# Kernel tuning notes

Measured on AMD Instinct MI355X. Metric: run time of the kernel, lower is better.

Reference implementation:

```python
import jax, jax.numpy as jnp
import numpy as np

B, L, V, E, H, DOUT = 32, 128, 30000, 300, 512, 5
NUM_STEPS = 5
WINDOW = 1


def setup_inputs() -> dict:
    key = jax.random.key(0)
    ks = jax.random.split(key, 16)
    def p(k, shape, scale=0.02):
        return jax.random.normal(k, shape, jnp.float32) * scale
    tokens = jax.random.randint(ks[0], (B, L), 1, V)
    lengths = jnp.maximum(jax.random.randint(ks[1], (B,), 1, L + 1), 8)
    embed = p(ks[2], (V, E), 0.1).at[0].set(0.0)  # padding_idx=0 row zeroed
    W0 = p(ks[3], (E, H)); b0 = jnp.zeros((H,), jnp.float32)
    Wg = p(ks[4], (3 * H + E + H, 7 * H)); bg = jnp.zeros((7 * H,), jnp.float32)
    Wgf = p(ks[5], (2 * H, H)); bgf = jnp.zeros((H,), jnp.float32)
    Wfi = p(ks[6], (2 * H, H)); bfi = jnp.zeros((H,), jnp.float32)
    Wgo = p(ks[7], (2 * H, H)); bgo = jnp.zeros((H,), jnp.float32)
    W1 = p(ks[8], (H, 2 * H)); b1 = jnp.zeros((2 * H,), jnp.float32)
    W2 = p(ks[9], (2 * H, DOUT)); b2 = jnp.zeros((DOUT,), jnp.float32)
    return dict(tokens=tokens, lengths=lengths, embed=embed, W0=W0, b0=b0,
                Wg=Wg, bg=bg, Wgf=Wgf, bgf=bgf, Wfi=Wfi, bfi=bfi,
                Wgo=Wgo, bgo=bgo, W1=W1, b1=b1, W2=W2, b2=b2)


def _shift_r(a, k):  # h_{i-k}
    return jnp.pad(a, ((0, 0), (k, 0), (0, 0)))[:, :L]


def _shift_l(a, k):  # h_{i+k}
    return jnp.pad(a, ((0, 0), (0, k), (0, 0)))[:, k:]


def reference(tokens, lengths, embed, W0, b0, Wg, bg, Wgf, bgf, Wfi, bfi,
              Wgo, bgo, W1, b1, W2, b2):
    x = embed[tokens]                                   # [B,L,E]
    mask = (jnp.arange(L)[None, :] < lengths[:, None]).astype(x.dtype)[:, :, None]
    lens = jnp.maximum(lengths.astype(x.dtype), 1.0)[:, None]  # [B,1]
    h = jnp.tanh(x @ W0 + b0) * mask                    # word node init [B,L,H]
    c = jnp.zeros_like(h)
    g = jnp.sum(h, axis=1) / lens                       # global node [B,H]
    cg = jnp.zeros_like(g)

    def step(carry, _):
        h, c, g, cg = carry
        hl = sum(_shift_r(h, k) for k in range(1, WINDOW + 1))
        hr = sum(_shift_l(h, k) for k in range(1, WINDOW + 1))
        gb = jnp.broadcast_to(g[:, None, :], h.shape)
        ctx = jnp.concatenate([hl, h, hr, x, gb], axis=-1)  # [B,L,3H+E+H]
        gates = ctx @ Wg + bg                               # [B,L,7H]
        gi, gl, gf, gr, gs, go, gu = jnp.split(gates, 7, axis=-1)
        nrm = jax.nn.softmax(jnp.stack([gi, gl, gf, gr, gs], 0), axis=0)
        i_, l_, f_, r_, s_ = nrm[0], nrm[1], nrm[2], nrm[3], nrm[4]
        o = jax.nn.sigmoid(go)
        u = jnp.tanh(gu)
        c_new = (l_ * _shift_r(c, 1) + f_ * c + r_ * _shift_l(c, 1)
                 + s_ * cg[:, None, :] + i_ * u) * mask
        h_new = o * jnp.tanh(c_new) * mask
        # global (sentence-state) node update
        h_avg = jnp.sum(h_new, axis=1) / lens
        gcat = jnp.concatenate([g, h_avg], axis=-1)         # [B,2H]
        fg = gcat @ Wgf + bgf                               # [B,H]
        og = jax.nn.sigmoid(gcat @ Wgo + bgo)
        fi = jnp.concatenate([jnp.broadcast_to(g[:, None, :], h_new.shape),
                              h_new], axis=-1) @ Wfi + bfi  # [B,L,H]
        slot_logits = jnp.concatenate([fg[:, None, :], fi], axis=1)  # [B,L+1,H]
        slot_mask = jnp.concatenate([jnp.ones((B, 1, 1), x.dtype), mask], axis=1)
        slot_logits = jnp.where(slot_mask > 0, slot_logits, -1e9)
        w = jax.nn.softmax(slot_logits, axis=1)
        cg_new = w[:, 0] * cg + jnp.sum(w[:, 1:] * c_new, axis=1)
        g_new = og * jnp.tanh(cg_new)
        return (h_new, c_new, g_new, cg_new), None

    (h, c, g, cg), _ = jax.lax.scan(step, (h, c, g, cg), None, length=NUM_STEPS)
    logits = jnp.tanh(g @ W1 + b1) @ W2 + b2            # [B,DOUT]
    return jax.nn.log_softmax(logits, axis=-1)
```

## Files before the change

### kernel.cpp

```cpp
#include <hip/hip_runtime.h>
#include <hip/hip_bf16.h>
#include <math.h>

#define B_ 32
#define L_ 128
#define LP 130
#define E_ 300
#define EP 320
#define H_ 512
#define DOUT_ 5
#define NSTEP 5
#define G7 3584
#define KGATES 1856
#define KFI 512

typedef __hip_bfloat16 bf16;
using bf16x8 = __attribute__((ext_vector_type(8))) __bf16;
using f32x4 = __attribute__((ext_vector_type(4))) float;

__device__ __forceinline__ void gload16(const void* g, void* l) {
  __builtin_amdgcn_global_load_lds(
      (const __attribute__((address_space(1))) void*)g,
      (__attribute__((address_space(3))) void*)l, 16, 0, 0);
}

__global__ void fill_zero(float* __restrict__ p, int n) {
  int i = blockIdx.x * blockDim.x + threadIdx.x;
  if (i < n) p[i] = 0.f;
}

__global__ void mask_lens_kernel(const int* __restrict__ lengths,
                                 float* __restrict__ maskf,
                                 float* __restrict__ invlens) {
  int i = blockIdx.x * blockDim.x + threadIdx.x;
  if (i < B_ * L_) {
    int b = i >> 7, l = i & 127;
    maskf[i] = (l < lengths[b]) ? 1.f : 0.f;
    if (l == 0) invlens[b] = 1.f / fmaxf((float)lengths[b], 1.f);
  }
}

__global__ void embed_bf16_kernel(const int* __restrict__ tokens,
                                  const float* __restrict__ embed,
                                  bf16* __restrict__ xb) {
  int i = blockIdx.x * blockDim.x + threadIdx.x;
  if (i >= B_ * L_ * EP) return;
  int e = i % EP, bl = i / EP;
  float v = (e < E_) ? embed[(size_t)tokens[bl] * E_ + e] : 0.f;
  xb[i] = __float2bfloat16(v);
}

__global__ void fill_pad(bf16* __restrict__ hpad) {
  int i = blockIdx.x * blockDim.x + threadIdx.x;
  if (i >= B_ * 2 * H_) return;
  int hh = i & (H_ - 1);
  int r = (i >> 9) & 1, b = i >> 10;
  hpad[((size_t)(b * LP + r * (LP - 1))) * H_ + hh] = __float2bfloat16(0.f);
}

__global__ __launch_bounds__(256) void transpose_to_bf16(
    const float* __restrict__ W, bf16* __restrict__ Wt, int Kreal, int Ncols,
    int dstStride) {
  __shared__ float tile[64][65];
  const int k0 = blockIdx.x * 64, n0 = blockIdx.y * 64;
  const int t = threadIdx.x;
  const int nn = t & 63, kk0 = t >> 6;
#pragma unroll
  for (int p = 0; p < 16; ++p) {
    int kk = kk0 + p * 4;
    int gk = k0 + kk;
    tile[kk][nn] = (gk < Kreal) ? W[(size_t)gk * Ncols + n0 + nn] : 0.f;
  }
  __syncthreads();
#pragma unroll
  for (int p = 0; p < 2; ++p) {
    int r = (t >> 3) + p * 32;
    int kb = (t & 7) * 8;
    union { ushort h[8]; uint4 v; } u;
#pragma unroll
    for (int e = 0; e < 8; ++e) {
      bf16 b = __float2bfloat16(tile[kb + e][r]);
      u.h[e] = *(ushort*)&b;
    }
    *(uint4*)&Wt[(size_t)(n0 + r) * dstStride + k0 + kb] = u.v;
  }
}

template <int AMAP, int OUTMODE>
__global__ __launch_bounds__(256) void gemm_mfma(
    const bf16* __restrict__ A, const bf16* __restrict__ X3,
    const bf16* __restrict__ Bt, const float* __restrict__ bias,
    const float* __restrict__ b2batch, const float* __restrict__ rowscale,
    void* __restrict__ Cout, int N, int KP, int act) {
  __shared__ ushort As[128 * 64];
  __shared__ ushort Bs[128 * 64];
  const int tid = threadIdx.x;
  const int lane = tid & 63;
  const int w = tid >> 6;
  const int wr = w >> 1, wc = w & 1;
  const int nbx = gridDim.x;
  const int nwg = nbx * gridDim.y;
  int id = blockIdx.y * nbx + blockIdx.x;
  if ((nwg & 7) == 0) { int q = nwg >> 3; id = (id & 7) * q + (id >> 3); }
  const int bxi = id % nbx, byi = id / nbx;
  const int rowBase = byi * 128, colBase = bxi * 128;
  const int l15 = lane & 15, l4 = lane >> 4;
  f32x4 acc[4][4] = {};

  const bf16* bP[4];
  const bf16* aP[4];
  const bf16* xP[4];
#pragma unroll
  for (int i = 0; i < 4; ++i) {
    int c = tid + 256 * i;
    int r = c >> 3;
    int ql = (c & 7) ^ (r & 7);
    bP[i] = Bt + (size_t)(colBase + r) * KP + ql * 8;
    if constexpr (AMAP == 0) {
      aP[i] = A + (size_t)(rowBase + r) * KP + ql * 8;
    } else {
      const int b = rowBase >> 7;
      aP[i] = A + ((size_t)(b * LP + r)) * H_ + ql * 8;
      xP[i] = X3 + (size_t)(rowBase + r) * EP + ql * 8;
    }
  }

  auto step_ = [&](const bf16* const* ap, int ko, int kb) {
#pragma unroll
    for (int i = 0; i < 4; ++i) {
      gload16(ap[i] + ko, &As[(tid + 256 * i) * 8]);
      gload16(bP[i] + kb, &Bs[(tid + 256 * i) * 8]);
    }
    __syncthreads();
#pragma unroll
    for (int kh = 0; kh < 2; ++kh) {
      bf16x8 aF[4], bF[4];
#pragma unroll
      for (int m = 0; m < 4; ++m) {
        int row = wr * 64 + m * 16 + l15;
        aF[m] = *(const bf16x8*)&As[row * 64 +
                                    (((kh << 2) + l4) ^ (l15 & 7)) * 8];
      }
#pragma unroll
      for (int n = 0; n < 4; ++n) {
        int row = wc * 64 + n * 16 + l15;
        bF[n] = *(const bf16x8*)&Bs[row * 64 +
                                    (((kh << 2) + l4) ^ (l15 & 7)) * 8];
      }
#pragma unroll
      for (int m = 0; m < 4; ++m)
#pragma unroll
        for (int n = 0; n < 4; ++n)
          acc[m][n] = __builtin_amdgcn_mfma_f32_16x16x32_bf16(
              aF[m], bF[n], acc[m][n], 0, 0, 0);
    }
    __syncthreads();
  };

  if constexpr (AMAP == 0) {
    const int nIter = KP >> 6;
    for (int t = 0; t < nIter; ++t) step_(aP, t * 64, t * 64);
  } else {
    for (int t = 0; t < 24; ++t) step_(aP, t * 64, t * 64);
    for (int t = 24; t < 29; ++t) step_(xP, (t - 24) * 64, t * 64);
  }

  const int bidx = rowBase >> 7;
#pragma unroll
  for (int m = 0; m < 4; ++m) {
#pragma unroll
    for (int n = 0; n < 4; ++n) {
      int col = colBase + wc * 64 + n * 16 + l15;
      float bv = bias[col];
      if (b2batch) bv += b2batch[(size_t)bidx * N + col];
      if constexpr (OUTMODE == 5) {
        bf16 tmp[4];
#pragma unroll
        for (int j = 0; j < 4; ++j)
          tmp[j] = __float2bfloat16(acc[m][n][j] + bv);
        int row0 = rowBase + wr * 64 + m * 16 + l4 * 4;
        *(uint2*)&((bf16*)Cout)[((size_t)(row0 >> 2) * N + col) * 4] =
            *(uint2*)tmp;
      } else {
#pragma unroll
        for (int j = 0; j < 4; ++j) {
          int row = rowBase + wr * 64 + m * 16 + l4 * 4 + j;
          float v = acc[m][n][j] + bv;
          if (act == 1) v = tanhf(v);
          v *= rowscale[row];
          size_t oi = ((size_t)((row >> 7) * LP + (row & 127) + 1)) * H_ + col;
          ((bf16*)Cout)[oi] = __float2bfloat16(v);
        }
      }
    }
  }
}

__global__ __launch_bounds__(256) void gvec_gemm(
    const float* __restrict__ g, const float* __restrict__ Wgg,
    const float* __restrict__ Wfi, float* __restrict__ gg,
    float* __restrict__ gfi) {
  __shared__ float vin[H_];
  __shared__ float red[4][64];
  const int b = blockIdx.y;
  for (int i = threadIdx.x; i < H_; i += 256) vin[i] = g[(size_t)b * H_ + i];
  __syncthreads();
  const int o = threadIdx.x & 63, kp = threadIdx.x >> 6;
  const bool isg = blockIdx.x < 56;
  const int n0 = isg ? blockIdx.x * 64 : (blockIdx.x - 56) * 64;
  const float* W = isg ? Wgg : Wfi;
  const int ldw = isg ? G7 : H_;
  float acc = 0.f;
#pragma unroll 4
  for (int k = kp * 128; k < kp * 128 + 128; ++k)
    acc = fmaf(vin[k], W[(size_t)k * ldw + n0 + o], acc);
  red[kp][o] = acc;
  __syncthreads();
  if (threadIdx.x < 64) {
    int t = threadIdx.x;
    float v = red[0][t] + red[1][t] + red[2][t] + red[3][t];
    if (isg) gg[(size_t)b * G7 + n0 + t] = v;
    else gfi[(size_t)b * H_ + n0 + t] = v;
  }
}

__global__ __launch_bounds__(256) void fi_slot_kernel(
    const bf16* __restrict__ hpad, const bf16* __restrict__ Wfit,
    const float* __restrict__ bfi, const float* __restrict__ gfi,
    const float* __restrict__ fg, const float* __restrict__ og,
    const float* __restrict__ c_new, const float* __restrict__ cg_old,
    const float* __restrict__ maskf, float* __restrict__ cg_new,
    float* __restrict__ g_new) {
  __shared__ __align__(16) char smem[64 * 129 * 4 + 3072];
  ushort* As = (ushort*)smem;
  ushort* Bs = As + 128 * 64;
  float* sfi = (float*)smem;
  float* part = sfi + 64 * 129;

  const int tid = threadIdx.x;
  const int lane = tid & 63;
  const int w = tid >> 6;
  const int b = blockIdx.y;
  const int colBase = blockIdx.x * 64;
  const int l15 = lane & 15, l4 = lane >> 4;
  f32x4 acc[2][4] = {};

  const bf16* aP[4];
  const bf16* bP[2];
#pragma unroll
  for (int i = 0; i < 4; ++i) {
    int c = tid + 256 * i;
    int r = c >> 3;
    int ql = (c & 7) ^ (r & 7);
    aP[i] = hpad + ((size_t)(b * LP + r + 1)) * H_ + ql * 8;
  }
#pragma unroll
  for (int i = 0; i < 2; ++i) {
    int c = tid + 256 * i;
    int r = c >> 3;
    int ql = (c & 7) ^ (r & 7);
    bP[i] = Wfit + (size_t)(colBase + r) * KFI + ql * 8;
  }

  for (int t = 0; t < 8; ++t) {
    int k0 = t * 64;
#pragma unroll
    for (int i = 0; i < 4; ++i)
      gload16(aP[i] + k0, &As[(tid + 256 * i) * 8]);
#pragma unroll
    for (int i = 0; i < 2; ++i)
      gload16(bP[i] + k0, &Bs[(tid + 256 * i) * 8]);
    __syncthreads();
#pragma unroll
    for (int kh = 0; kh < 2; ++kh) {
      bf16x8 aF[2], bF[4];
#pragma unroll
      for (int m = 0; m < 2; ++m) {
        int row = w * 32 + m * 16 + l15;
        aF[m] = *(const bf16x8*)&As[row * 64 +
                                    (((kh << 2) + l4) ^ (l15 & 7)) * 8];
      }
#pragma unroll
      for (int n = 0; n < 4; ++n) {
        int row = n * 16 + l15;
        bF[n] = *(const bf16x8*)&Bs[row * 64 +
                                    (((kh << 2) + l4) ^ (l15 & 7)) * 8];
      }
#pragma unroll
      for (int m = 0; m < 2; ++m)
#pragma unroll
        for (int n = 0; n < 4; ++n)
          acc[m][n] = __builtin_amdgcn_mfma_f32_16x16x32_bf16(
              aF[m], bF[n], acc[m][n], 0, 0, 0);
    }
    __syncthreads();
  }

#pragma unroll
  for (int m = 0; m < 2; ++m) {
#pragma unroll
    for (int n = 0; n < 4; ++n) {
      int hl_ = n * 16 + l15;
      float bv = bfi[colBase + hl_] + gfi[(size_t)b * H_ + colBase + hl_];
#pragma unroll
      for (int j = 0; j < 4; ++j) {
        int l = w * 32 + m * 16 + l4 * 4 + j;
        sfi[hl_ * 129 + l] = acc[m][n][j] + bv;
      }
    }
  }
  __syncthreads();

  {
    int h = tid & 63, q = tid >> 6;
    int hcol = colBase + h;
    const float* mp = maskf + b * L_;
    float m = -3.0e38f, s = 0.f, tv = 0.f;
    for (int l = q * 32; l < q * 32 + 32; ++l) {
      if (mp[l] > 0.f) {
        float xv = sfi[h * 129 + l];
        float vv = c_new[((size_t)(b * L_ + l)) * H_ + hcol];
        float m2 = fmaxf(m, xv);
        float sc = expf(m - m2);
        float e = expf(xv - m2);
        s = s * sc + e;
        tv = tv * sc + e * vv;
        m = m2;
      }
    }
    part[q * 192 + h] = m;
    part[q * 192 + 64 + h] = s;
    part[q * 192 + 128 + h] = tv;
  }
  __syncthreads();
  if (tid < 64) {
    int hcol = colBase + tid;
    int i0 = b * H_ + hcol;
    float mm = part[tid], s0 = part[64 + tid], t0 = part[128 + tid];
#pragma unroll
    for (int k = 1; k < 4; ++k) {
      float mk = part[k * 192 + tid];
      float m2 = fmaxf(mm, mk);
      float e1 = expf(mm - m2), e2 = expf(mk - m2);
      s0 = s0 * e1 + part[k * 192 + 64 + tid] * e2;
      t0 = t0 * e1 + part[k * 192 + 128 + tid] * e2;
      mm = m2;
    }
    float f = fg[i0];
    float m2 = fmaxf(mm, f);
    float ea = expf(mm - m2), eb = expf(f - m2);
    s0 = s0 * ea + eb;
    t0 = t0 * ea + cg_old[i0] * eb;
    float cgn = t0 / s0;
    float gn = og[i0] * tanhf(cgn);
    cg_new[i0] = cgn;
    g_new[i0] = gn;
  }
}

__global__ __launch_bounds__(512) void cell_mean_kernel(
    const bf16* __restrict__ gates, const float* __restrict__ c_old,
    const float* __restrict__ cg_old, const float* __restrict__ maskf,
    const float* __restrict__ invlens, bf16* __restrict__ hpad,
    float* __restrict__ c_new, float* __restrict__ havg) {
  __shared__ float part[8][64];
  const int b = blockIdx.y;
  const int h0 = blockIdx.x * 64;
  const int hh = threadIdx.x & 63;
  const int lq = threadIdx.x >> 6;
  const int hcol = h0 + hh;
  const float cgv = cg_old[b * H_ + hcol];
  float s = 0.f;
  for (int it = 0; it < 4; ++it) {
    const int gi = it * 8 + lq;
    const int l0 = gi * 4;
    const size_t gbase = ((size_t)(b * 32 + gi) * G7 + hcol) * 4;
    uint2 gv[7];
#pragma unroll
    for (int gt = 0; gt < 7; ++gt)
      gv[gt] = *(const uint2*)&gates[gbase + (size_t)gt * H_ * 4];
    float crow[6];
#pragma unroll
    for (int jj = 0; jj < 6; ++jj) {
      int l = l0 + jj - 1;
      crow[jj] = (l >= 0 && l < L_)
                     ? c_old[((size_t)(b * L_ + l)) * H_ + hcol]
                     : 0.f;
    }
#pragma unroll
    for (int j = 0; j < 4; ++j) {
      int l = l0 + j;
      int bl = b * L_ + l;
      float gl_[7];
#pragma unroll
      for (int gt = 0; gt < 7; ++gt) {
        ushort us = ((const ushort*)&gv[gt])[j];
        bf16 hb;
        *(ushort*)&hb = us;
        gl_[gt] = __bfloat162float(hb);
      }
      float m = fmaxf(fmaxf(fmaxf(gl_[0], gl_[1]), fmaxf(gl_[2], gl_[3])),
                      gl_[4]);
      float ei = expf(gl_[0] - m), el = expf(gl_[1] - m),
            ef = expf(gl_[2] - m), er = expf(gl_[3] - m),
            es = expf(gl_[4] - m);
      float inv = 1.f / (ei + el + ef + er + es);
      float o = 1.f / (1.f + expf(-gl_[5]));
      float u = tanhf(gl_[6]);
      float mk = maskf[bl];
      float cn = (el * crow[j] + ef * crow[j + 1] + er * crow[j + 2] +
                  es * cgv + ei * u) * inv * mk;
      float hn = o * tanhf(cn) * mk;
      c_new[(size_t)bl * H_ + hcol] = cn;
      hpad[((size_t)(b * LP + l + 1)) * H_ + hcol] = __float2bfloat16(hn);
      s += hn;
    }
  }
  part[lq][hh] = s;
  __syncthreads();
  if (threadIdx.x < 64) {
    int t = threadIdx.x;
    float v = 0.f;
#pragma unroll
    for (int k = 0; k < 8; ++k) v += part[k][t];
    havg[b * H_ + h0 + t] = v * invlens[b];
  }
}

__global__ __launch_bounds__(256) void reduce_mean_v2(
    const bf16* __restrict__ hpad, const float* __restrict__ invlens,
    float* __restrict__ outf) {
  __shared__ float sm[4][64];
  int b = blockIdx.y, h0 = blockIdx.x * 64;
  int lg = threadIdx.x >> 6, hh = threadIdx.x & 63;
  float s = 0.f;
  for (int l = lg * 32; l < lg * 32 + 32; ++l)
    s += __bfloat162float(hpad[((size_t)(b * LP + l + 1)) * H_ + h0 + hh]);
  sm[lg][hh] = s;
  __syncthreads();
  if (threadIdx.x < 64) {
    int t = threadIdx.x;
    outf[b * H_ + h0 + t] =
        (sm[0][t] + sm[1][t] + sm[2][t] + sm[3][t]) * invlens[b];
  }
}

__global__ __launch_bounds__(256) void batch_vec_gemm(
    const float* __restrict__ in1, int K1, const float* __restrict__ in2,
    int K2, const float* __restrict__ Wa, const float* __restrict__ ba,
    float* __restrict__ outa, int acta, const float* __restrict__ Wb,
    const float* __restrict__ bb, float* __restrict__ outb, int actb, int N) {
  const float* W = (blockIdx.z == 0) ? Wa : Wb;
  const float* bias = (blockIdx.z == 0) ? ba : bb;
  float* op = (blockIdx.z == 0) ? outa : outb;
  int act = (blockIdx.z == 0) ? acta : actb;
  __shared__ float vin[1024];
  __shared__ float red[4][64];
  const int K = K1 + K2;
  const int n0 = blockIdx.x * 64, b = blockIdx.y;
  for (int i = threadIdx.x; i < K; i += 256)
    vin[i] = (i < K1) ? in1[(size_t)b * K1 + i]
                      : in2[(size_t)b * K2 + (i - K1)];
  __syncthreads();
  const int o = threadIdx.x & 63, kp = threadIdx.x >> 6;
  float acc = 0.f;
  const int kc = K >> 2;
#pragma unroll 4
  for (int k = kp * kc; k < kp * kc + kc; ++k)
    acc = fmaf(vin[k], W[(size_t)k * N + n0 + o], acc);
  red[kp][o] = acc;
  __syncthreads();
  if (threadIdx.x < 64) {
    int t = threadIdx.x;
    float v = red[0][t] + red[1][t] + red[2][t] + red[3][t] + bias[n0 + t];
    if (act == 1) v = 1.f / (1.f + expf(-v));
    else if (act == 2) v = tanhf(v);
    op[(size_t)b * N + n0 + t] = v;
  }
}

__global__ __launch_bounds__(256) void final_head_kernel(
    const float* __restrict__ g, const float* __restrict__ W1,
    const float* __restrict__ b1, const float* __restrict__ W2,
    const float* __restrict__ b2, float* __restrict__ out) {
  __shared__ float gv[H_];
  __shared__ float t1s[2 * H_];
  __shared__ float red[256][6];
  const int b = blockIdx.x;
  const int tid = threadIdx.x;
  for (int i = tid; i < H_; i += 256) gv[i] = g[b * H_ + i];
  __syncthreads();
  float accp[4];
#pragma unroll
  for (int p = 0; p < 4; ++p) accp[p] = b1[tid + p * 256];
  for (int k = 0; k < H_; ++k) {
    float gk = gv[k];
#pragma unroll
    for (int p = 0; p < 4; ++p)
      accp[p] = fmaf(gk, W1[(size_t)k * (2 * H_) + tid + p * 256], accp[p]);
  }
#pragma unroll
  for (int p = 0; p < 4; ++p) t1s[tid + p * 256] = tanhf(accp[p]);
  __syncthreads();
  float pd[DOUT_] = {0.f, 0.f, 0.f, 0.f, 0.f};
#pragma unroll
  for (int p = 0; p < 4; ++p) {
    int j = tid + p * 256;
    float tv = t1s[j];
#pragma unroll
    for (int d = 0; d < DOUT_; ++d)
      pd[d] = fmaf(tv, W2[(size_t)j * DOUT_ + d], pd[d]);
  }
#pragma unroll
  for (int d = 0; d < DOUT_; ++d) red[tid][d] = pd[d];
  __syncthreads();
  for (int stride = 128; stride >= 1; stride >>= 1) {
    if (tid < stride) {
#pragma unroll
      for (int d = 0; d < DOUT_; ++d) red[tid][d] += red[tid + stride][d];
    }
    __syncthreads();
  }
  if (tid == 0) {
    float lg[DOUT_];
#pragma unroll
    for (int d = 0; d < DOUT_; ++d) lg[d] = red[0][d] + b2[d];
    float m = lg[0];
#pragma unroll
    for (int d = 1; d < DOUT_; ++d) m = fmaxf(m, lg[d]);
    float s = 0.f;
#pragma unroll
    for (int d = 0; d < DOUT_; ++d) s += expf(lg[d] - m);
    float ls = logf(s);
#pragma unroll
    for (int d = 0; d < DOUT_; ++d) out[b * DOUT_ + d] = lg[d] - m - ls;
  }
}

extern "C" void kernel_launch(void* const* d_in, const int* in_sizes, int n_in,
                              void* d_out, int out_size, void* d_ws,
                              size_t ws_size, hipStream_t stream) {
  (void)in_sizes; (void)n_in; (void)out_size; (void)ws_size;
  const int* tokens = (const int*)d_in[0];
  const int* lengths = (const int*)d_in[1];
  const float* embed = (const float*)d_in[2];
  const float* W0 = (const float*)d_in[3];
  const float* b0 = (const float*)d_in[4];
  const float* Wg = (const float*)d_in[5];
  const float* bg = (const float*)d_in[6];
  const float* Wgf = (const float*)d_in[7];
  const float* bgf = (const float*)d_in[8];
  const float* Wfi = (const float*)d_in[9];
  const float* bfi = (const float*)d_in[10];
  const float* Wgo = (const float*)d_in[11];
  const float* bgo = (const float*)d_in[12];
  const float* W1 = (const float*)d_in[13];
  const float* b1 = (const float*)d_in[14];
  const float* W2 = (const float*)d_in[15];
  const float* b2 = (const float*)d_in[16];
  float* out = (float*)d_out;

  float* ws = (float*)d_ws;
  size_t off = 0;
  auto alloc = [&](size_t nf) {
    float* p = ws + off;
    off += (nf + 7) & ~(size_t)7;
    return p;
  };
  bf16* xb = (bf16*)alloc((size_t)B_ * L_ * EP / 2);
  float* maskf = alloc(B_ * L_);
  float* invlens = alloc(B_);
  bf16* hpad = (bf16*)alloc((size_t)B_ * LP * H_ / 2);
  float* cb0 = alloc((size_t)B_ * L_ * H_);
  float* cb1 = alloc((size_t)B_ * L_ * H_);
  float* g = alloc(B_ * H_);
  float* cgb0 = alloc(B_ * H_);
  float* cgb1 = alloc(B_ * H_);
  float* havg = alloc(B_ * H_);
  float* fg = alloc(B_ * H_);
  float* og = alloc(B_ * H_);
  float* gg = alloc((size_t)B_ * G7);
  float* gfi = alloc(B_ * H_);
  bf16* gatesb = (bf16*)alloc((size_t)B_ * L_ * G7 / 2);
  bf16* Wgt = (bf16*)alloc((size_t)G7 * KGATES / 2);
  bf16* W0t = (bf16*)alloc((size_t)H_ * EP / 2);
  bf16* Wfit = (bf16*)alloc((size_t)H_ * KFI / 2);

  mask_lens_kernel<<<(B_ * L_ + 255) / 256, 256, 0, stream>>>(lengths, maskf,
                                                              invlens);
  embed_bf16_kernel<<<(B_ * L_ * EP + 255) / 256, 256, 0, stream>>>(tokens,
                                                                    embed, xb);
  transpose_to_bf16<<<dim3(24, G7 / 64), 256, 0, stream>>>(Wg, Wgt, 1536, G7,
                                                           KGATES);
  transpose_to_bf16<<<dim3(5, G7 / 64), 256, 0, stream>>>(
      Wg + (size_t)1536 * G7, Wgt + 1536, 300, G7, KGATES);
  transpose_to_bf16<<<dim3(5, H_ / 64), 256, 0, stream>>>(W0, W0t, 300, H_, EP);
  transpose_to_bf16<<<dim3(8, H_ / 64), 256, 0, stream>>>(
      Wfi + (size_t)H_ * H_, Wfit, H_, H_, KFI);
  fill_pad<<<(B_ * 2 * H_ + 255) / 256, 256, 0, stream>>>(hpad);
  gemm_mfma<0, 3><<<dim3(H_ / 128, (B_ * L_) / 128), 256, 0, stream>>>(
      xb, nullptr, W0t, b0, nullptr, maskf, hpad, H_, EP, 1);
  reduce_mean_v2<<<dim3(8, B_), 256, 0, stream>>>(hpad, invlens, g);
  fill_zero<<<(B_ * L_ * H_ + 255) / 256, 256, 0, stream>>>(cb0, B_ * L_ * H_);
  fill_zero<<<(B_ * H_ + 255) / 256, 256, 0, stream>>>(cgb0, B_ * H_);

  float* cb[2] = {cb0, cb1};
  float* cgb[2] = {cgb0, cgb1};
  int cur = 0;
  for (int step = 0; step < NSTEP; ++step) {
    int nxt = cur ^ 1;
    gvec_gemm<<<dim3(64, B_), 256, 0, stream>>>(g, Wg + (size_t)1836 * G7,
                                                Wfi, gg, gfi);
    gemm_mfma<2, 5><<<dim3(G7 / 128, (B_ * L_) / 128), 256, 0, stream>>>(
        hpad, xb, Wgt, bg, gg, nullptr, gatesb, G7, KGATES, 0);
    cell_mean_kernel<<<dim3(H_ / 64, B_), 512, 0, stream>>>(
        gatesb, cb[cur], cgb[cur], maskf, invlens, hpad, cb[nxt], havg);
    batch_vec_gemm<<<dim3(8, B_, 2), 256, 0, stream>>>(
        g, H_, havg, H_, Wgf, bgf, fg, 0, Wgo, bgo, og, 1, H_);
    fi_slot_kernel<<<dim3(H_ / 64, B_), 256, 0, stream>>>(
        hpad, Wfit, bfi, gfi, fg, og, cb[nxt], cgb[cur], maskf, cgb[nxt], g);
    cur = nxt;
  }
  final_head_kernel<<<B_, 256, 0, stream>>>(g, W1, b1, W2, b2, out);
}
```

Measured before the change: 823.0 us.

## Split gates GEMM into 64-row tiles, skip padded halves, store cell state in bf16

```diff
diff --git a/kernel.cpp b/kernel.cpp
--- a/kernel.cpp
+++ b/kernel.cpp
@@ -86,12 +86,10 @@
   }
 }
 
-template <int AMAP, int OUTMODE>
-__global__ __launch_bounds__(256) void gemm_mfma(
-    const bf16* __restrict__ A, const bf16* __restrict__ X3,
-    const bf16* __restrict__ Bt, const float* __restrict__ bias,
-    const float* __restrict__ b2batch, const float* __restrict__ rowscale,
-    void* __restrict__ Cout, int N, int KP, int act) {
+__global__ __launch_bounds__(256) void gemm_mfma_init(
+    const bf16* __restrict__ A, const bf16* __restrict__ Bt,
+    const float* __restrict__ bias, const float* __restrict__ rowscale,
+    bf16* __restrict__ Cout, int N, int KP) {
   __shared__ ushort As[128 * 64];
   __shared__ ushort Bs[128 * 64];
   const int tid = threadIdx.x;
@@ -109,27 +107,22 @@
 
   const bf16* bP[4];
   const bf16* aP[4];
-  const bf16* xP[4];
 #pragma unroll
   for (int i = 0; i < 4; ++i) {
     int c = tid + 256 * i;
     int r = c >> 3;
     int ql = (c & 7) ^ (r & 7);
     bP[i] = Bt + (size_t)(colBase + r) * KP + ql * 8;
-    if constexpr (AMAP == 0) {
-      aP[i] = A + (size_t)(rowBase + r) * KP + ql * 8;
-    } else {
-      const int b = rowBase >> 7;
-      aP[i] = A + ((size_t)(b * LP + r)) * H_ + ql * 8;
-      xP[i] = X3 + (size_t)(rowBase + r) * EP + ql * 8;
-    }
-  }
-
-  auto step_ = [&](const bf16* const* ap, int ko, int kb) {
+    aP[i] = A + (size_t)(rowBase + r) * KP + ql * 8;
+  }
+
+  const int nIter = KP >> 6;
+  for (int t = 0; t < nIter; ++t) {
+    int k0 = t * 64;
 #pragma unroll
     for (int i = 0; i < 4; ++i) {
-      gload16(ap[i] + ko, &As[(tid + 256 * i) * 8]);
-      gload16(bP[i] + kb, &Bs[(tid + 256 * i) * 8]);
+      gload16(aP[i] + k0, &As[(tid + 256 * i) * 8]);
+      gload16(bP[i] + k0, &Bs[(tid + 256 * i) * 8]);
     }
     __syncthreads();
 #pragma unroll
@@ -155,43 +148,114 @@
               aF[m], bF[n], acc[m][n], 0, 0, 0);
     }
     __syncthreads();
-  };
-
-  if constexpr (AMAP == 0) {
-    const int nIter = KP >> 6;
-    for (int t = 0; t < nIter; ++t) step_(aP, t * 64, t * 64);
-  } else {
-    for (int t = 0; t < 24; ++t) step_(aP, t * 64, t * 64);
-    for (int t = 24; t < 29; ++t) step_(xP, (t - 24) * 64, t * 64);
-  }
-
-  const int bidx = rowBase >> 7;
+  }
+
 #pragma unroll
   for (int m = 0; m < 4; ++m) {
 #pragma unroll
     for (int n = 0; n < 4; ++n) {
       int col = colBase + wc * 64 + n * 16 + l15;
       float bv = bias[col];
-      if (b2batch) bv += b2batch[(size_t)bidx * N + col];
-      if constexpr (OUTMODE == 5) {
-        bf16 tmp[4];
-#pragma unroll
-        for (int j = 0; j < 4; ++j)
-          tmp[j] = __float2bfloat16(acc[m][n][j] + bv);
-        int row0 = rowBase + wr * 64 + m * 16 + l4 * 4;
-        *(uint2*)&((bf16*)Cout)[((size_t)(row0 >> 2) * N + col) * 4] =
-            *(uint2*)tmp;
-      } else {
-#pragma unroll
-        for (int j = 0; j < 4; ++j) {
-          int row = rowBase + wr * 64 + m * 16 + l4 * 4 + j;
-          float v = acc[m][n][j] + bv;
-          if (act == 1) v = tanhf(v);
-          v *= rowscale[row];
-          size_t oi = ((size_t)((row >> 7) * LP + (row & 127) + 1)) * H_ + col;
-          ((bf16*)Cout)[oi] = __float2bfloat16(v);
-        }
-      }
+#pragma unroll
+      for (int j = 0; j < 4; ++j) {
+        int row = rowBase + wr * 64 + m * 16 + l4 * 4 + j;
+        float v = tanhf(acc[m][n][j] + bv) * rowscale[row];
+        size_t oi = ((size_t)((row >> 7) * LP + (row & 127) + 1)) * H_ + col;
+        Cout[oi] = __float2bfloat16(v);
+      }
+    }
+  }
+}
+
+__global__ __launch_bounds__(256) void gates_gemm(
+    const bf16* __restrict__ hpad, const bf16* __restrict__ xb,
+    const bf16* __restrict__ Wgt, const float* __restrict__ bias,
+    const float* __restrict__ gg, const int* __restrict__ lengths,
+    bf16* __restrict__ gatesb) {
+  __shared__ ushort As[64 * 64];
+  __shared__ ushort Bs[128 * 64];
+  const int tid = threadIdx.x;
+  const int lane = tid & 63;
+  const int w = tid >> 6;
+  int id = blockIdx.y * 28 + blockIdx.x;
+  id = (id & 7) * 224 + (id >> 3);
+  const int bxi = id % 28, byi = id / 28;
+  const int b = byi >> 1, lhalf = byi & 1;
+  if (lhalf && lengths[b] <= 64) return;
+  const int rowBase = byi * 64;
+  const int colBase = bxi * 128;
+  const int l15 = lane & 15, l4 = lane >> 4;
+  f32x4 acc[4][2] = {};
+
+  const int hRowBase = b * LP + lhalf * 64;
+  const int blBase = b * L_ + lhalf * 64;
+  const bf16* aP[2];
+  const bf16* xP[2];
+  const bf16* bP[4];
+#pragma unroll
+  for (int i = 0; i < 2; ++i) {
+    int c = tid + 256 * i;
+    int r = c >> 3;
+    int ql = (c & 7) ^ (r & 7);
+    aP[i] = hpad + (size_t)(hRowBase + r) * H_ + ql * 8;
+    xP[i] = xb + (size_t)(blBase + r) * EP + ql * 8;
+  }
+#pragma unroll
+  for (int i = 0; i < 4; ++i) {
+    int c = tid + 256 * i;
+    int r = c >> 3;
+    int ql = (c & 7) ^ (r & 7);
+    bP[i] = Wgt + (size_t)(colBase + r) * KGATES + ql * 8;
+  }
+
+  auto step_ = [&](const bf16* const* ap, int ko, int kb) {
+#pragma unroll
+    for (int i = 0; i < 2; ++i)
+      gload16(ap[i] + ko, &As[(tid + 256 * i) * 8]);
+#pragma unroll
+    for (int i = 0; i < 4; ++i)
+      gload16(bP[i] + kb, &Bs[(tid + 256 * i) * 8]);
+    __syncthreads();
+#pragma unroll
+    for (int kh = 0; kh < 2; ++kh) {
+      bf16x8 aF[4], bF[2];
+#pragma unroll
+      for (int m = 0; m < 4; ++m) {
+        int row = m * 16 + l15;
+        aF[m] = *(const bf16x8*)&As[row * 64 +
+                                    (((kh << 2) + l4) ^ (l15 & 7)) * 8];
+      }
+#pragma unroll
+      for (int n = 0; n < 2; ++n) {
+        int row = w * 32 + n * 16 + l15;
+        bF[n] = *(const bf16x8*)&Bs[row * 64 +
+                                    (((kh << 2) + l4) ^ (l15 & 7)) * 8];
+      }
+#pragma unroll
+      for (int m = 0; m < 4; ++m)
+#pragma unroll
+        for (int n = 0; n < 2; ++n)
+          acc[m][n] = __builtin_amdgcn_mfma_f32_16x16x32_bf16(
+              aF[m], bF[n], acc[m][n], 0, 0, 0);
+    }
+    __syncthreads();
+  };
+
+  for (int t = 0; t < 24; ++t) step_(aP, t * 64, t * 64);
+  for (int t = 24; t < 29; ++t) step_(xP, (t - 24) * 64, t * 64);
+
+#pragma unroll
+  for (int m = 0; m < 4; ++m) {
+#pragma unroll
+    for (int n = 0; n < 2; ++n) {
+      int col = colBase + w * 32 + n * 16 + l15;
+      float bv = bias[col] + gg[(size_t)b * G7 + col];
+      bf16 tmp[4];
+#pragma unroll
+      for (int j = 0; j < 4; ++j)
+        tmp[j] = __float2bfloat16(acc[m][n][j] + bv);
+      int row0 = rowBase + m * 16 + l4 * 4;
+      *(uint2*)&gatesb[((size_t)(row0 >> 2) * G7 + col) * 4] = *(uint2*)tmp;
     }
   }
 }
@@ -228,7 +292,7 @@
     const bf16* __restrict__ hpad, const bf16* __restrict__ Wfit,
     const float* __restrict__ bfi, const float* __restrict__ gfi,
     const float* __restrict__ fg, const float* __restrict__ og,
-    const float* __restrict__ c_new, const float* __restrict__ cg_old,
+    const bf16* __restrict__ c_new, const float* __restrict__ cg_old,
     const float* __restrict__ maskf, float* __restrict__ cg_new,
     float* __restrict__ g_new) {
   __shared__ __align__(16) char smem[64 * 129 * 4 + 3072];
@@ -319,7 +383,7 @@
     for (int l = q * 32; l < q * 32 + 32; ++l) {
       if (mp[l] > 0.f) {
         float xv = sfi[h * 129 + l];
-        float vv = c_new[((size_t)(b * L_ + l)) * H_ + hcol];
+        float vv = __bfloat162float(c_new[((size_t)(b * L_ + l)) * H_ + hcol]);
         float m2 = fmaxf(m, xv);
         float sc = expf(m - m2);
         float e = expf(xv - m2);
@@ -359,10 +423,10 @@
 }
 
 __global__ __launch_bounds__(512) void cell_mean_kernel(
-    const bf16* __restrict__ gates, const float* __restrict__ c_old,
+    const bf16* __restrict__ gates, const bf16* __restrict__ c_old,
     const float* __restrict__ cg_old, const float* __restrict__ maskf,
     const float* __restrict__ invlens, bf16* __restrict__ hpad,
-    float* __restrict__ c_new, float* __restrict__ havg) {
+    bf16* __restrict__ c_new, float* __restrict__ havg) {
   __shared__ float part[8][64];
   const int b = blockIdx.y;
   const int h0 = blockIdx.x * 64;
@@ -384,7 +448,7 @@
     for (int jj = 0; jj < 6; ++jj) {
       int l = l0 + jj - 1;
       crow[jj] = (l >= 0 && l < L_)
-                     ? c_old[((size_t)(b * L_ + l)) * H_ + hcol]
+                     ? __bfloat162float(c_old[((size_t)(b * L_ + l)) * H_ + hcol])
                      : 0.f;
     }
 #pragma unroll
@@ -411,7 +475,7 @@
       float cn = (el * crow[j] + ef * crow[j + 1] + er * crow[j + 2] +
                   es * cgv + ei * u) * inv * mk;
       float hn = o * tanhf(cn) * mk;
-      c_new[(size_t)bl * H_ + hcol] = cn;
+      c_new[(size_t)bl * H_ + hcol] = __float2bfloat16(cn);
       hpad[((size_t)(b * LP + l + 1)) * H_ + hcol] = __float2bfloat16(hn);
       s += hn;
     }
@@ -571,8 +635,8 @@
   float* maskf = alloc(B_ * L_);
   float* invlens = alloc(B_);
   bf16* hpad = (bf16*)alloc((size_t)B_ * LP * H_ / 2);
-  float* cb0 = alloc((size_t)B_ * L_ * H_);
-  float* cb1 = alloc((size_t)B_ * L_ * H_);
+  bf16* cb0 = (bf16*)alloc((size_t)B_ * L_ * H_ / 2);
+  bf16* cb1 = (bf16*)alloc((size_t)B_ * L_ * H_ / 2);
   float* g = alloc(B_ * H_);
   float* cgb0 = alloc(B_ * H_);
   float* cgb1 = alloc(B_ * H_);
@@ -598,21 +662,22 @@
   transpose_to_bf16<<<dim3(8, H_ / 64), 256, 0, stream>>>(
       Wfi + (size_t)H_ * H_, Wfit, H_, H_, KFI);
   fill_pad<<<(B_ * 2 * H_ + 255) / 256, 256, 0, stream>>>(hpad);
-  gemm_mfma<0, 3><<<dim3(H_ / 128, (B_ * L_) / 128), 256, 0, stream>>>(
-      xb, nullptr, W0t, b0, nullptr, maskf, hpad, H_, EP, 1);
+  gemm_mfma_init<<<dim3(H_ / 128, (B_ * L_) / 128), 256, 0, stream>>>(
+      xb, W0t, b0, maskf, hpad, H_, EP);
   reduce_mean_v2<<<dim3(8, B_), 256, 0, stream>>>(hpad, invlens, g);
-  fill_zero<<<(B_ * L_ * H_ + 255) / 256, 256, 0, stream>>>(cb0, B_ * L_ * H_);
+  fill_zero<<<(B_ * L_ * H_ / 2 + 255) / 256, 256, 0, stream>>>(
+      (float*)cb0, B_ * L_ * H_ / 2);
   fill_zero<<<(B_ * H_ + 255) / 256, 256, 0, stream>>>(cgb0, B_ * H_);
 
-  float* cb[2] = {cb0, cb1};
+  bf16* cb[2] = {cb0, cb1};
   float* cgb[2] = {cgb0, cgb1};
   int cur = 0;
   for (int step = 0; step < NSTEP; ++step) {
     int nxt = cur ^ 1;
     gvec_gemm<<<dim3(64, B_), 256, 0, stream>>>(g, Wg + (size_t)1836 * G7,
                                                 Wfi, gg, gfi);
-    gemm_mfma<2, 5><<<dim3(G7 / 128, (B_ * L_) / 128), 256, 0, stream>>>(
-        hpad, xb, Wgt, bg, gg, nullptr, gatesb, G7, KGATES, 0);
+    gates_gemm<<<dim3(28, 64), 256, 0, stream>>>(hpad, xb, Wgt, bg, gg,
+                                                 lengths, gatesb);
     cell_mean_kernel<<<dim3(H_ / 64, B_), 512, 0, stream>>>(
         gatesb, cb[cur], cgb[cur], maskf, invlens, hpad, cb[nxt], havg);
     batch_vec_gemm<<<dim3(8, B_, 2), 256, 0, stream>>>(
```

Result: faster. 765.5 us (-7.0%).
